# Performance work log

Measured on AMD Instinct MI355X. Metric: run time of the kernel, lower is better.

Reference implementation:

```python
import jax, jax.numpy as jnp
import numpy as np

B, S, D = 2, 2048, 1024
H, DK, DV = 16, 64, 64
DF = 4096
EPS = 1e-5


def _layer_norm(x, g, b):
    mu = jnp.mean(x, axis=-1, keepdims=True)
    var = jnp.mean((x - mu) ** 2, axis=-1, keepdims=True)
    return (x - mu) * jax.lax.rsqrt(var + EPS) * g + b


def setup_inputs() -> dict:
    key = jax.random.key(0)
    ks = jax.random.split(key, 12)
    s = lambda fan_in: 1.0 / np.sqrt(fan_in)
    return {
        "enc_input": jax.random.normal(ks[0], (B, S, D), dtype=jnp.float32),
        "wq": jax.random.uniform(ks[1], (D, H * DK), jnp.float32, -s(D), s(D)),
        "wk": jax.random.uniform(ks[2], (D, H * DK), jnp.float32, -s(D), s(D)),
        "wv": jax.random.uniform(ks[3], (D, H * DV), jnp.float32, -s(D), s(D)),
        "wo": jax.random.uniform(ks[4], (H * DV, D), jnp.float32, -s(H * DV), s(H * DV)),
        "w1": jax.random.uniform(ks[5], (D, DF), jnp.float32, -s(D), s(D)),
        "b1": jax.random.uniform(ks[6], (DF,), jnp.float32, -s(D), s(D)),
        "w2": jax.random.uniform(ks[7], (DF, D), jnp.float32, -s(DF), s(DF)),
        "b2": jax.random.uniform(ks[8], (D,), jnp.float32, -s(DF), s(DF)),
        "ln1_g": jnp.ones((D,), jnp.float32),
        "ln1_b": jnp.zeros((D,), jnp.float32),
        "ln2_g": jnp.ones((D,), jnp.float32),
        "ln2_b": jnp.zeros((D,), jnp.float32),
    }


def reference(enc_input, wq, wk, wv, wo, w1, b1, w2, b2, ln1_g, ln1_b, ln2_g, ln2_b):
    x = enc_input
    # QKV projections -> [B, H, S, d]
    q = (x @ wq).reshape(B, S, H, DK).transpose(0, 2, 1, 3)
    k = (x @ wk).reshape(B, S, H, DK).transpose(0, 2, 1, 3)
    v = (x @ wv).reshape(B, S, H, DV).transpose(0, 2, 1, 3)
    # scaled dot-product attention (scale = 1/sqrt(d_k), dropout is identity at eval)
    score = jnp.einsum("bhqd,bhkd->bhqk", q, k) / jnp.sqrt(jnp.float32(DK))
    attn = jax.nn.softmax(score, axis=-1)
    ctx = jnp.einsum("bhqk,bhkd->bhqd", attn, v)
    ctx = ctx.transpose(0, 2, 1, 3).reshape(B, S, H * DV)
    atn_out = ctx @ wo
    # Add & Norm 1
    h = _layer_norm(x + atn_out, ln1_g, ln1_b)
    # FFN
    ffn = jax.nn.relu(h @ w1 + b1) @ w2 + b2
    # Add & Norm 2
    return _layer_norm(h + ffn, ln2_g, ln2_b)
```

## Files before the change

### kernel.cpp

```cpp
#include <hip/hip_runtime.h>
#include <hip/hip_bf16.h>

typedef __bf16 bf16;
typedef __bf16 bf16x4 __attribute__((ext_vector_type(4)));
typedef __bf16 bf16x8 __attribute__((ext_vector_type(8)));
typedef float  f32x4  __attribute__((ext_vector_type(4)));

#define KB 2
#define KS 2048
#define KD 1024
#define KH 16
#define KM (KB*KS)
#define KQKVN 3072
#define KDF 4096

__device__ __forceinline__ f32x4 mfma16(bf16x8 a, bf16x8 b, f32x4 c) {
  return __builtin_amdgcn_mfma_f32_16x16x32_bf16(a, b, c, 0, 0, 0);
}

__device__ __forceinline__ float exp2_hw(float x) {
  float r;
  asm("v_exp_f32 %0, %1" : "=v"(r) : "v"(x));
  return r;
}

__device__ __forceinline__ void g2l16(const bf16* g, bf16* l) {
  __builtin_amdgcn_global_load_lds(
      (const __attribute__((address_space(1))) unsigned int*)g,
      (__attribute__((address_space(3))) unsigned int*)l, 16, 0, 0);
}

__global__ __launch_bounds__(256) void cvt_bf16_kernel(const float* __restrict__ in,
                                                       bf16* __restrict__ out, int n) {
  int i = (blockIdx.x * 256 + threadIdx.x) * 4;
  if (i >= n) return;
  f32x4 v = *reinterpret_cast<const f32x4*>(in + i);
  bf16x4 o;
  o[0] = (bf16)v[0]; o[1] = (bf16)v[1]; o[2] = (bf16)v[2]; o[3] = (bf16)v[3];
  *reinterpret_cast<bf16x4*>(out + i) = o;
}

__global__ __launch_bounds__(256) void wtrans_kernel(const float* __restrict__ W,
                                                     bf16* __restrict__ WT,
                                                     int K, int N) {
  __shared__ float tile[32][33];
  const int n0 = blockIdx.x * 32, k0 = blockIdx.y * 32;
  const int tx = threadIdx.x & 31, ty = threadIdx.x >> 5;
#pragma unroll
  for (int j = ty; j < 32; j += 8) tile[j][tx] = W[(size_t)(k0 + j) * N + n0 + tx];
  __syncthreads();
#pragma unroll
  for (int j = ty; j < 32; j += 8) WT[(size_t)(n0 + j) * K + k0 + tx] = (bf16)tile[tx][j];
}

__global__ __launch_bounds__(256) void kvpack_kernel(const bf16* __restrict__ qkv,
                                                     bf16* __restrict__ kp,
                                                     bf16* __restrict__ vt) {
  __shared__ bf16 tile[64][72];
  const int s0 = blockIdx.x * 64;
  const int bh = blockIdx.y;
  const int b = bh >> 4, h = bh & 15;
  const int t = threadIdx.x;
  const int r = t >> 3, c8 = (t & 7) * 8;
#pragma unroll
  for (int rr = r; rr < 64; rr += 32) {
    const size_t grow = (size_t)(b * KS + s0 + rr) * KQKVN + h * 64 + c8;
    bf16x8 kv = *reinterpret_cast<const bf16x8*>(&qkv[grow + 1024]);
    *reinterpret_cast<bf16x8*>(&kp[((size_t)bh * KS + s0 + rr) * 64 + c8]) = kv;
    bf16x8 vv = *reinterpret_cast<const bf16x8*>(&qkv[grow + 2048]);
#pragma unroll
    for (int j = 0; j < 8; j++) tile[rr][c8 + j] = vv[j];
  }
  __syncthreads();
#pragma unroll
  for (int dd = r; dd < 64; dd += 32) {
    bf16x8 v;
#pragma unroll
    for (int j = 0; j < 8; j++) {
      const int pi = c8 + j;
      const int key = ((pi >> 5) << 5) | (((pi >> 2) & 1) << 4) |
                      (((pi >> 3) & 3) << 2) | (pi & 3);
      v[j] = tile[key][dd];
    }
    *reinterpret_cast<bf16x8*>(&vt[(size_t)bh * 64 * KS + (size_t)dd * KS + s0 + c8]) = v;
  }
}

struct P4 { bf16* p[4]; };

template <typename OUT_T, bool RELU, bool HAS_BIAS, bool SPLITK>
__global__ __launch_bounds__(512, 2) void gemm256(const bf16* __restrict__ A,
                                                  const bf16* __restrict__ BT,
                                                  OUT_T* __restrict__ C, P4 pr,
                                                  const float* __restrict__ bias,
                                                  int M, int N, int K, int Kslice) {
  extern __shared__ __align__(16) bf16 sm[];
  const int tid = threadIdx.x, lane = tid & 63, w = tid >> 6;
  const int wr = w >> 2, wc = w & 3;
  const int gx = gridDim.x;
  const int nwg = gx * gridDim.y;
  int flat = blockIdx.y * gx + blockIdx.x;
  flat = (flat & 7) * (nwg >> 3) + (flat >> 3);
  const int bn = (flat % gx) * 256;
  const int bm = (flat / gx) * 256;
  const int z = blockIdx.z;
  const int NT = (SPLITK ? Kslice : K) >> 5;
  const int lr = lane & 15, hi = lane >> 4;
  int srow[2], scol[2];
#pragma unroll
  for (int j = 0; j < 2; j++) {
    const int u = j * 512 + tid;
    srow[j] = u >> 2;
    scol[j] = (((u & 3) ^ ((u >> 2) & 3))) * 8;
  }
  const bf16* Abase = A + (size_t)bm * K + (SPLITK ? z * Kslice : 0);
  const bf16* Bbase = BT + (size_t)bn * K + (SPLITK ? z * Kslice : 0);
  auto stage = [&](int t) {
    bf16* dst = sm + (size_t)(t & 3) * 16384;
    const int k0 = t * 32;
#pragma unroll
    for (int j = 0; j < 2; j++) {
      g2l16(Abase + (size_t)srow[j] * K + k0 + scol[j], dst + (j * 512 + w * 64) * 8);
      g2l16(Bbase + (size_t)srow[j] * K + k0 + scol[j],
            dst + 8192 + (j * 512 + w * 64) * 8);
    }
  };
  f32x4 acc[8][4] = {};
  stage(0); stage(1); stage(2);
  for (int t = 0; t < NT; t++) {
    const int rem = NT - 1 - t;
    if (rem >= 2)      asm volatile("s_waitcnt vmcnt(8)" ::: "memory");
    else if (rem == 1) asm volatile("s_waitcnt vmcnt(4)" ::: "memory");
    else               asm volatile("s_waitcnt vmcnt(0)" ::: "memory");
    __builtin_amdgcn_sched_barrier(0);
    __builtin_amdgcn_s_barrier();
    __builtin_amdgcn_sched_barrier(0);
    if (t + 3 < NT) stage(t + 3);
    const bf16* sa = sm + (size_t)(t & 3) * 16384;
    const bf16* sb = sa + 8192;
    bf16x8 af[8], bfr[4];
#pragma unroll
    for (int mf = 0; mf < 8; mf++) {
      const int row = wr * 128 + mf * 16 + lr;
      af[mf] = *(const bf16x8*)&sa[row * 32 + ((hi ^ (row & 3)) * 8)];
    }
#pragma unroll
    for (int nf = 0; nf < 4; nf++) {
      const int row = wc * 64 + nf * 16 + lr;
      bfr[nf] = *(const bf16x8*)&sb[row * 32 + ((hi ^ (row & 3)) * 8)];
    }
    __builtin_amdgcn_s_setprio(1);
#pragma unroll
    for (int mf = 0; mf < 8; mf++)
#pragma unroll
      for (int nf = 0; nf < 4; nf++)
        acc[mf][nf] = mfma16(af[mf], bfr[nf], acc[mf][nf]);
    __builtin_amdgcn_s_setprio(0);
  }
  const int rg = hi * 4, cl = lr;
  if (SPLITK) {
    bf16* P = pr.p[z];
#pragma unroll
    for (int mf = 0; mf < 8; mf++)
#pragma unroll
      for (int nf = 0; nf < 4; nf++) {
        const int col = bn + wc * 64 + nf * 16 + cl;
#pragma unroll
        for (int i = 0; i < 4; i++) {
          const int row = bm + wr * 128 + mf * 16 + rg + i;
          P[(size_t)row * N + col] = (bf16)acc[mf][nf][i];
        }
      }
  } else {
#pragma unroll
    for (int mf = 0; mf < 8; mf++)
#pragma unroll
      for (int nf = 0; nf < 4; nf++) {
        const int col = bn + wc * 64 + nf * 16 + cl;
        float bv = 0.f;
        if (HAS_BIAS) bv = bias[col];
#pragma unroll
        for (int i = 0; i < 4; i++) {
          const int row = bm + wr * 128 + mf * 16 + rg + i;
          float v = acc[mf][nf][i] + bv;
          if (RELU) v = fmaxf(v, 0.f);
          C[(size_t)row * N + col] = (OUT_T)v;
        }
      }
  }
}

template <typename OUT_T, bool RELU, bool HAS_BIAS, int BN>
__global__ __launch_bounds__(256) void gemm_bt(const bf16* __restrict__ A,
                                               const bf16* __restrict__ BT,
                                               OUT_T* __restrict__ C,
                                               const float* __restrict__ bias,
                                               int M, int N, int K) {
  constexpr int NF = BN / 32;
  __shared__ __align__(16) bf16 sa[2][128 * 32];
  __shared__ __align__(16) bf16 sb[2][BN * 32];
  const int t = threadIdx.x, lane = t & 63, w = t >> 6;
  const int gx = gridDim.x;
  const int nwg = gx * gridDim.y;
  int flat = blockIdx.y * gx + blockIdx.x;
  if ((nwg & 7) == 0) flat = (flat & 7) * (nwg >> 3) + (flat >> 3);
  const int bn = (flat % gx) * BN;
  const int bm = (flat / gx) * 128;
  const int wr = w >> 1, wc = w & 1;
  const int wcol = wc * (BN / 2);
  const int lr = lane & 15, lk = (lane >> 4) * 8;
  const int srow = w * 16 + (lane >> 2);
  const int scol = (lane & 3) * 8;
  f32x4 acc[4][NF] = {};
  const int NT = K >> 5;
  auto stage = [&](int kt, int buf) {
#pragma unroll
    for (int i = 0; i < 2; i++)
      g2l16(A + (size_t)(bm + i * 64 + srow) * K + kt * 32 + scol,
            &sa[buf][(i * 64 + w * 16) * 32]);
#pragma unroll
    for (int i = 0; i < BN / 64; i++)
      g2l16(BT + (size_t)(bn + i * 64 + srow) * K + kt * 32 + scol,
            &sb[buf][(i * 64 + w * 16) * 32]);
  };
  stage(0, 0);
  int cur = 0;
  for (int kt = 0; kt < NT; kt++) {
    __syncthreads();
    if (kt + 1 < NT) stage(kt + 1, cur ^ 1);
    bf16x8 af[4], bfr[NF];
#pragma unroll
    for (int m = 0; m < 4; m++)
      af[m] = *(const bf16x8*)&sa[cur][(wr * 64 + m * 16 + lr) * 32 + lk];
#pragma unroll
    for (int n = 0; n < NF; n++)
      bfr[n] = *(const bf16x8*)&sb[cur][(wcol + n * 16 + lr) * 32 + lk];
#pragma unroll
    for (int m = 0; m < 4; m++)
#pragma unroll
      for (int n = 0; n < NF; n++)
        acc[m][n] = mfma16(af[m], bfr[n], acc[m][n]);
    cur ^= 1;
  }
  const int rg = (lane >> 4) * 4, cl = lane & 15;
#pragma unroll
  for (int m = 0; m < 4; m++)
#pragma unroll
    for (int n = 0; n < NF; n++) {
      const int col = bn + wcol + n * 16 + cl;
      float bv = 0.f;
      if (HAS_BIAS) bv = bias[col];
#pragma unroll
      for (int i = 0; i < 4; i++) {
        const int row = bm + wr * 64 + m * 16 + rg + i;
        float v = acc[m][n][i] + bv;
        if (RELU) v = fmaxf(v, 0.f);
        C[(size_t)row * N + col] = (OUT_T)v;
      }
    }
}

__global__ __launch_bounds__(256) void attn_kernel(const bf16* __restrict__ qkv,
                                                   const bf16* __restrict__ kp,
                                                   const bf16* __restrict__ vt,
                                                   bf16* __restrict__ ctx) {
  __shared__ __align__(16) bf16 ksm[3][64 * 64];
  __shared__ __align__(16) bf16 vsm[3][64 * 64];
  const int t = threadIdx.x, lane = t & 63, w = t >> 6;
  const int flat = blockIdx.y * 16 + blockIdx.x;
  const int xcd = flat & 7, jj = flat >> 3;
  const int bh = xcd + 8 * (jj >> 4);
  const int qb = jj & 15;
  const int b = bh >> 4, h = bh & 15;
  const int qbase = qb * 128 + w * 32;
  const int lr = lane & 15, hi = lane >> 4;
  const int lk = hi * 8, rg = hi * 4, cl = lr;

  bf16x8 aq[2][2];
#pragma unroll
  for (int m = 0; m < 2; m++)
#pragma unroll
    for (int kk = 0; kk < 2; kk++) {
      bf16x8 v = *reinterpret_cast<const bf16x8*>(
          &qkv[(size_t)(b * KS + qbase + m * 16 + lr) * KQKVN + h * 64 + kk * 32 + lk]);
#pragma unroll
      for (int e = 0; e < 8; e++) v[e] = (bf16)((float)v[e] * 0.18033688f);
      aq[m][kk] = v;
    }
  bf16x8 ones;
#pragma unroll
  for (int j = 0; j < 8; j++) ones[j] = (bf16)1.0f;

  const bf16* kpb = kp + (size_t)bh * KS * 64;
  const bf16* vtb = vt + (size_t)bh * 64 * KS;

  auto stageKV = [&](int tt) {
    const int kt0 = tt * 64;
    const int buf = tt % 3;
    bf16* kd = &ksm[buf][0];
    bf16* vd = &vsm[buf][0];
#pragma unroll
    for (int i = 0; i < 2; i++) {
      const int q = i * 4096 + w * 1024 + (lane << 4);
      const int row = q >> 7;
      const int slot = ((q >> 4) & 7) ^ (row & 7);
      g2l16(kpb + (size_t)(kt0 + row) * 64 + slot * 8, kd + ((i * 4096 + w * 1024) >> 1));
      g2l16(vtb + (size_t)row * KS + kt0 + slot * 8,   vd + ((i * 4096 + w * 1024) >> 1));
    }
  };

  f32x4 accd[2][4] = {};
  f32x4 lsumv[2] = {};

  stageKV(0); stageKV(1);
  const int NT = KS / 64;
  for (int tt = 0; tt < NT; tt++) {
    if (tt < NT - 1) asm volatile("s_waitcnt vmcnt(4)" ::: "memory");
    else             asm volatile("s_waitcnt vmcnt(0)" ::: "memory");
    __builtin_amdgcn_sched_barrier(0);
    __builtin_amdgcn_s_barrier();
    __builtin_amdgcn_sched_barrier(0);
    if (tt + 2 < NT) stageKV(tt + 2);
    const int buf = tt % 3;
    const char* kb = (const char*)&ksm[buf][0];
    const char* vb = (const char*)&vsm[buf][0];
    bf16x8 bk[4][2];
#pragma unroll
    for (int n = 0; n < 4; n++)
#pragma unroll
      for (int kk = 0; kk < 2; kk++) {
        const int row = n * 16 + lr;
        bk[n][kk] = *(const bf16x8*)(kb + row * 128 +
                                     ((kk * 64 + hi * 16) ^ ((row & 7) << 4)));
      }
    f32x4 sc[2][4] = {};
    __builtin_amdgcn_s_setprio(1);
#pragma unroll
    for (int m = 0; m < 2; m++)
#pragma unroll
      for (int n = 0; n < 4; n++)
#pragma unroll
        for (int kk = 0; kk < 2; kk++)
          sc[m][n] = mfma16(bk[n][kk], aq[m][kk], sc[m][n]);
    __builtin_amdgcn_s_setprio(0);
    bf16x8 pa[2][2];
#pragma unroll
    for (int m = 0; m < 2; m++) {
      float p[4][4];
#pragma unroll
      for (int n = 0; n < 4; n++)
#pragma unroll
        for (int i = 0; i < 4; i++)
          p[n][i] = exp2_hw(sc[m][n][i]);
#pragma unroll
      for (int kk = 0; kk < 2; kk++) {
        bf16x8 v;
#pragma unroll
        for (int j = 0; j < 8; j++) v[j] = (bf16)p[kk * 2 + (j >> 2)][j & 3];
        pa[m][kk] = v;
      }
    }
    bf16x8 bv[4][2];
#pragma unroll
    for (int dt = 0; dt < 4; dt++)
#pragma unroll
      for (int kk = 0; kk < 2; kk++) {
        const int row = dt * 16 + lr;
        bv[dt][kk] = *(const bf16x8*)(vb + row * 128 +
                                      ((kk * 64 + hi * 16) ^ ((row & 7) << 4)));
      }
    __builtin_amdgcn_s_setprio(1);
#pragma unroll
    for (int m = 0; m < 2; m++) {
#pragma unroll
      for (int dt = 0; dt < 4; dt++)
#pragma unroll
        for (int kk = 0; kk < 2; kk++)
          accd[m][dt] = mfma16(pa[m][kk], bv[dt][kk], accd[m][dt]);
      lsumv[m] = mfma16(pa[m][0], ones, lsumv[m]);
      lsumv[m] = mfma16(pa[m][1], ones, lsumv[m]);
    }
    __builtin_amdgcn_s_setprio(0);
  }
#pragma unroll
  for (int m = 0; m < 2; m++)
#pragma unroll
    for (int dt = 0; dt < 4; dt++)
#pragma unroll
      for (int i = 0; i < 4; i++)
        ctx[(size_t)(b * KS + qbase + m * 16 + rg + i) * KD + h * 64 + dt * 16 + cl] =
            (bf16)(accd[m][dt][i] / lsumv[m][i]);
}

template <bool ABF, bool OBF>
__global__ __launch_bounds__(256) void ln_kernel(const void* __restrict__ aptr,
                                                 const float* __restrict__ bsum,
                                                 const float* __restrict__ g,
                                                 const float* __restrict__ bet,
                                                 void* __restrict__ outp) {
  const int row = blockIdx.x;
  const int t = threadIdx.x;
  const int lane = t & 63, wid = t >> 6;
  float v[4];
  {
    f32x4 bv = *reinterpret_cast<const f32x4*>(&bsum[(size_t)row * KD + t * 4]);
    if (ABF) {
      bf16x4 av = *reinterpret_cast<const bf16x4*>(
          (const bf16*)aptr + (size_t)row * KD + t * 4);
#pragma unroll
      for (int j = 0; j < 4; j++) v[j] = (float)av[j] + bv[j];
    } else {
      f32x4 av = *reinterpret_cast<const f32x4*>(
          (const float*)aptr + (size_t)row * KD + t * 4);
#pragma unroll
      for (int j = 0; j < 4; j++) v[j] = av[j] + bv[j];
    }
  }
  float s = 0.f, s2 = 0.f;
#pragma unroll
  for (int j = 0; j < 4; j++) { s += v[j]; s2 += v[j] * v[j]; }
#pragma unroll
  for (int off = 32; off; off >>= 1) {
    s += __shfl_xor(s, off, 64);
    s2 += __shfl_xor(s2, off, 64);
  }
  __shared__ float red[8];
  if (lane == 0) { red[wid] = s; red[wid + 4] = s2; }
  __syncthreads();
  s = red[0] + red[1] + red[2] + red[3];
  s2 = red[4] + red[5] + red[6] + red[7];
  const float mu = s * (1.f / KD);
  const float var = s2 * (1.f / KD) - mu * mu;
  const float rs = rsqrtf(var + 1e-5f);
  if (OBF) {
    bf16x4 o;
#pragma unroll
    for (int j = 0; j < 4; j++)
      o[j] = (bf16)((v[j] - mu) * rs * g[t * 4 + j] + bet[t * 4 + j]);
    *reinterpret_cast<bf16x4*>((bf16*)outp + (size_t)row * KD + t * 4) = o;
  } else {
    f32x4 o;
#pragma unroll
    for (int j = 0; j < 4; j++)
      o[j] = (v[j] - mu) * rs * g[t * 4 + j] + bet[t * 4 + j];
    *reinterpret_cast<f32x4*>((float*)outp + (size_t)row * KD + t * 4) = o;
  }
}

__global__ __launch_bounds__(256) void ln2_fused_kernel(const bf16* __restrict__ hh,
                                                        const bf16* __restrict__ p0,
                                                        const bf16* __restrict__ p1,
                                                        const bf16* __restrict__ p2,
                                                        const bf16* __restrict__ p3,
                                                        const float* __restrict__ b2,
                                                        const float* __restrict__ g,
                                                        const float* __restrict__ bet,
                                                        float* __restrict__ outp) {
  const int row = blockIdx.x;
  const int t = threadIdx.x;
  const int lane = t & 63, wid = t >> 6;
  const size_t base = (size_t)row * KD + t * 4;
  bf16x4 hv = *(const bf16x4*)(hh + base);
  bf16x4 a0 = *(const bf16x4*)(p0 + base);
  bf16x4 a1 = *(const bf16x4*)(p1 + base);
  bf16x4 a2 = *(const bf16x4*)(p2 + base);
  bf16x4 a3 = *(const bf16x4*)(p3 + base);
  f32x4 bv = *(const f32x4*)(b2 + t * 4);
  float v[4];
#pragma unroll
  for (int j = 0; j < 4; j++)
    v[j] = (float)hv[j] + (float)a0[j] + (float)a1[j] + (float)a2[j] + (float)a3[j] + bv[j];
  float s = 0.f, s2 = 0.f;
#pragma unroll
  for (int j = 0; j < 4; j++) { s += v[j]; s2 += v[j] * v[j]; }
#pragma unroll
  for (int off = 32; off; off >>= 1) {
    s += __shfl_xor(s, off, 64);
    s2 += __shfl_xor(s2, off, 64);
  }
  __shared__ float red[8];
  if (lane == 0) { red[wid] = s; red[wid + 4] = s2; }
  __syncthreads();
  s = red[0] + red[1] + red[2] + red[3];
  s2 = red[4] + red[5] + red[6] + red[7];
  const float mu = s * (1.f / KD);
  const float var = s2 * (1.f / KD) - mu * mu;
  const float rs = rsqrtf(var + 1e-5f);
  f32x4 o;
#pragma unroll
  for (int j = 0; j < 4; j++)
    o[j] = (v[j] - mu) * rs * g[t * 4 + j] + bet[t * 4 + j];
  *reinterpret_cast<f32x4*>(outp + base) = o;
}

extern "C" void kernel_launch(void* const* d_in, const int* in_sizes, int n_in,
                              void* d_out, int out_size, void* d_ws, size_t ws_size,
                              hipStream_t stream) {
  const float* x     = (const float*)d_in[0];
  const float* wq    = (const float*)d_in[1];
  const float* wk    = (const float*)d_in[2];
  const float* wv    = (const float*)d_in[3];
  const float* wo    = (const float*)d_in[4];
  const float* w1    = (const float*)d_in[5];
  const float* b1    = (const float*)d_in[6];
  const float* w2    = (const float*)d_in[7];
  const float* b2    = (const float*)d_in[8];
  const float* ln1g  = (const float*)d_in[9];
  const float* ln1b  = (const float*)d_in[10];
  const float* ln2g  = (const float*)d_in[11];
  const float* ln2b  = (const float*)d_in[12];
  float* out = (float*)d_out;

  char* ws = (char*)d_ws;
  bf16*  x_bf   = (bf16*)(ws + 0);
  bf16*  wqkvT  = (bf16*)(ws + 8388608);
  bf16*  woT    = (bf16*)(ws + 14680064);
  bf16*  w1T    = (bf16*)(ws + 16777216);
  bf16*  w2T    = (bf16*)(ws + 25165824);
  bf16*  qkv    = (bf16*)(ws + 33554432);
  bf16*  kp     = (bf16*)(ws + 58720256);
  bf16*  vt     = (bf16*)(ws + 67108864);
  float* proj   = (float*)(ws + 75497472);
  bf16*  ctx    = x_bf;
  bf16*  h_bf   = (bf16*)(ws + 8388608);
  bf16*  ffn1   = qkv;
  P4 pr;
  pr.p[0] = (bf16*)(ws + 0);
  pr.p[1] = (bf16*)(ws + 16777216);
  pr.p[2] = (bf16*)(ws + 67108864);
  pr.p[3] = (bf16*)(ws + 75497472);
  P4 pzero = {};

  cvt_bf16_kernel<<<dim3(KM * KD / 1024), 256, 0, stream>>>(x, x_bf, KM * KD);
  wtrans_kernel<<<dim3(32, 32), 256, 0, stream>>>(wq, wqkvT, KD, KD);
  wtrans_kernel<<<dim3(32, 32), 256, 0, stream>>>(wk, wqkvT + 1024 * 1024, KD, KD);
  wtrans_kernel<<<dim3(32, 32), 256, 0, stream>>>(wv, wqkvT + 2048 * 1024, KD, KD);
  wtrans_kernel<<<dim3(32, 32), 256, 0, stream>>>(wo, woT, KD, KD);
  wtrans_kernel<<<dim3(128, 32), 256, 0, stream>>>(w1, w1T, KD, KDF);
  wtrans_kernel<<<dim3(32, 128), 256, 0, stream>>>(w2, w2T, KDF, KD);

  gemm256<bf16, false, false, false>
      <<<dim3(KQKVN / 256, KM / 256, 1), 512, 131072, stream>>>(
      x_bf, wqkvT, qkv, pzero, nullptr, KM, KQKVN, KD, KD);

  kvpack_kernel<<<dim3(KS / 64, KB * KH), 256, 0, stream>>>(qkv, kp, vt);

  attn_kernel<<<dim3(KS / 128, KB * KH), 256, 0, stream>>>(qkv, kp, vt, ctx);

  gemm_bt<float, false, false, 64><<<dim3(KD / 64, KM / 128), 256, 0, stream>>>(
      ctx, woT, proj, nullptr, KM, KD, KD);

  ln_kernel<false, true><<<dim3(KM), 256, 0, stream>>>(x, proj, ln1g, ln1b, h_bf);

  gemm256<bf16, true, true, false>
      <<<dim3(KDF / 256, KM / 256, 1), 512, 131072, stream>>>(
      h_bf, w1T, ffn1, pzero, b1, KM, KDF, KD, KD);

  gemm256<bf16, false, false, true>
      <<<dim3(KD / 256, KM / 256, 4), 512, 131072, stream>>>(
      ffn1, w2T, (bf16*)nullptr, pr, nullptr, KM, KD, KDF, KDF / 4);

  ln2_fused_kernel<<<dim3(KM), 256, 0, stream>>>(
      h_bf, pr.p[0], pr.p[1], pr.p[2], pr.p[3], b2, ln2g, ln2b, out);
}
```

Baseline: 241.7 us.

## Batch weight transposes into fewer launches and deepen attention KV pipeline

Merges the six weight transpose/convert launches into two launches: one with a z-dimension over the four 1024x1024 weights, and one covering w1 and w2 with swapped block indexing for w2. The attention kernel's K/V shared-memory ring grows from 3 to 4 buffers and prefetches three tiles ahead, with the vmcnt waits adjusted to match. This cuts launch overhead and is meant to hide more global-load latency in attention, at the cost of more LDS per block, which may lower occupancy.

Result: faster. 228.4 us (-5.5%).

```diff
diff --git a/kernel.cpp b/kernel.cpp
--- a/kernel.cpp
+++ b/kernel.cpp
@@ -40,11 +40,35 @@
   *reinterpret_cast<bf16x4*>(out + i) = o;
 }
 
-__global__ __launch_bounds__(256) void wtrans_kernel(const float* __restrict__ W,
-                                                     bf16* __restrict__ WT,
-                                                     int K, int N) {
+struct WT4 { const float* src[4]; bf16* dst[4]; };
+
+__global__ __launch_bounds__(256) void wtrans4_kernel(WT4 jobs) {
   __shared__ float tile[32][33];
+  const float* W = jobs.src[blockIdx.z];
+  bf16* WT = jobs.dst[blockIdx.z];
   const int n0 = blockIdx.x * 32, k0 = blockIdx.y * 32;
+  const int tx = threadIdx.x & 31, ty = threadIdx.x >> 5;
+#pragma unroll
+  for (int j = ty; j < 32; j += 8) tile[j][tx] = W[(size_t)(k0 + j) * 1024 + n0 + tx];
+  __syncthreads();
+#pragma unroll
+  for (int j = ty; j < 32; j += 8)
+    WT[(size_t)(n0 + j) * 1024 + k0 + tx] = (bf16)tile[tx][j];
+}
+
+__global__ __launch_bounds__(256) void wtrans_big_kernel(const float* __restrict__ w1,
+                                                         bf16* __restrict__ w1T,
+                                                         const float* __restrict__ w2,
+                                                         bf16* __restrict__ w2T) {
+  __shared__ float tile[32][33];
+  const float* W; bf16* WT; int K, N, n0, k0;
+  if (blockIdx.z == 0) {
+    W = w1; WT = w1T; K = 1024; N = 4096;
+    n0 = blockIdx.x * 32; k0 = blockIdx.y * 32;
+  } else {
+    W = w2; WT = w2T; K = 4096; N = 1024;
+    n0 = blockIdx.y * 32; k0 = blockIdx.x * 32;
+  }
   const int tx = threadIdx.x & 31, ty = threadIdx.x >> 5;
 #pragma unroll
   for (int j = ty; j < 32; j += 8) tile[j][tx] = W[(size_t)(k0 + j) * N + n0 + tx];
@@ -264,8 +288,8 @@
                                                    const bf16* __restrict__ kp,
                                                    const bf16* __restrict__ vt,
                                                    bf16* __restrict__ ctx) {
-  __shared__ __align__(16) bf16 ksm[3][64 * 64];
-  __shared__ __align__(16) bf16 vsm[3][64 * 64];
+  __shared__ __align__(16) bf16 ksm[4][64 * 64];
+  __shared__ __align__(16) bf16 vsm[4][64 * 64];
   const int t = threadIdx.x, lane = t & 63, w = t >> 6;
   const int flat = blockIdx.y * 16 + blockIdx.x;
   const int xcd = flat & 7, jj = flat >> 3;
@@ -296,9 +320,8 @@
 
   auto stageKV = [&](int tt) {
     const int kt0 = tt * 64;
-    const int buf = tt % 3;
-    bf16* kd = &ksm[buf][0];
-    bf16* vd = &vsm[buf][0];
+    bf16* kd = &ksm[tt & 3][0];
+    bf16* vd = &vsm[tt & 3][0];
 #pragma unroll
     for (int i = 0; i < 2; i++) {
       const int q = i * 4096 + w * 1024 + (lane << 4);
@@ -312,18 +335,19 @@
   f32x4 accd[2][4] = {};
   f32x4 lsumv[2] = {};
 
-  stageKV(0); stageKV(1);
+  stageKV(0); stageKV(1); stageKV(2);
   const int NT = KS / 64;
   for (int tt = 0; tt < NT; tt++) {
-    if (tt < NT - 1) asm volatile("s_waitcnt vmcnt(4)" ::: "memory");
-    else             asm volatile("s_waitcnt vmcnt(0)" ::: "memory");
+    const int rem = NT - 1 - tt;
+    if (rem >= 2)      asm volatile("s_waitcnt vmcnt(8)" ::: "memory");
+    else if (rem == 1) asm volatile("s_waitcnt vmcnt(4)" ::: "memory");
+    else               asm volatile("s_waitcnt vmcnt(0)" ::: "memory");
     __builtin_amdgcn_sched_barrier(0);
     __builtin_amdgcn_s_barrier();
     __builtin_amdgcn_sched_barrier(0);
-    if (tt + 2 < NT) stageKV(tt + 2);
-    const int buf = tt % 3;
-    const char* kb = (const char*)&ksm[buf][0];
-    const char* vb = (const char*)&vsm[buf][0];
+    if (tt + 3 < NT) stageKV(tt + 3);
+    const char* kb = (const char*)&ksm[tt & 3][0];
+    const char* vb = (const char*)&vsm[tt & 3][0];
     bf16x8 bk[4][2];
 #pragma unroll
     for (int n = 0; n < 4; n++)
@@ -532,12 +556,14 @@
   P4 pzero = {};
 
   cvt_bf16_kernel<<<dim3(KM * KD / 1024), 256, 0, stream>>>(x, x_bf, KM * KD);
-  wtrans_kernel<<<dim3(32, 32), 256, 0, stream>>>(wq, wqkvT, KD, KD);
-  wtrans_kernel<<<dim3(32, 32), 256, 0, stream>>>(wk, wqkvT + 1024 * 1024, KD, KD);
-  wtrans_kernel<<<dim3(32, 32), 256, 0, stream>>>(wv, wqkvT + 2048 * 1024, KD, KD);
-  wtrans_kernel<<<dim3(32, 32), 256, 0, stream>>>(wo, woT, KD, KD);
-  wtrans_kernel<<<dim3(128, 32), 256, 0, stream>>>(w1, w1T, KD, KDF);
-  wtrans_kernel<<<dim3(32, 128), 256, 0, stream>>>(w2, w2T, KDF, KD);
+  WT4 jobs;
+  jobs.src[0] = wq; jobs.src[1] = wk; jobs.src[2] = wv; jobs.src[3] = wo;
+  jobs.dst[0] = wqkvT;
+  jobs.dst[1] = wqkvT + 1024 * 1024;
+  jobs.dst[2] = wqkvT + 2048 * 1024;
+  jobs.dst[3] = woT;
+  wtrans4_kernel<<<dim3(32, 32, 4), 256, 0, stream>>>(jobs);
+  wtrans_big_kernel<<<dim3(128, 32, 2), 256, 0, stream>>>(w1, w1T, w2, w2T);
 
   gemm256<bf16, false, false, false>
       <<<dim3(KQKVN / 256, KM / 256, 1), 512, 131072, stream>>>(
```
